# Performance work log

Measured on AMD Instinct MI355X. Metric: run time of the kernel, lower is better.

## Reference

```python
import jax, jax.numpy as jnp
import numpy as np

B, S, HIST = 2, 2048, 2048
H, HK, D = 16, 16, 128
DIM = H * D

def setup_inputs() -> dict:
    key = jax.random.key(0)
    ks = jax.random.split(key, 8)
    x = jax.random.normal(ks[0], (B, S, DIM), jnp.float32)
    prev_k = jax.random.normal(ks[1], (B, HIST, HK, D), jnp.float32)
    prev_v = jax.random.normal(ks[2], (B, HIST, HK, D), jnp.float32)
    # causal mask: history fully visible, causal within the current chunk
    q_pos = HIST + jnp.arange(S)
    k_pos = jnp.arange(HIST + S)
    mask = jnp.where(k_pos[None, :] <= q_pos[:, None], 0.0, -1e9).astype(jnp.float32)[None, None]
    sc = 0.02
    wq = jax.random.normal(ks[3], (DIM, DIM), jnp.float32) * sc
    wk = jax.random.normal(ks[4], (DIM, DIM), jnp.float32) * sc
    wv = jax.random.normal(ks[5], (DIM, DIM), jnp.float32) * sc
    wo = jax.random.normal(ks[6], (DIM, DIM), jnp.float32) * sc
    return {"x": x, "prev_k": prev_k, "prev_v": prev_v, "mask": mask,
            "wq": wq, "wk": wk, "wv": wv, "wo": wo}

def reference(x, prev_k, prev_v, mask, wq, wk, wv, wo):
    b, s, _ = x.shape
    # nn.Linear: y = x @ W^T, weights stored [out, in]
    xq = jnp.einsum('bsd,ed->bse', x, wq).reshape(b, s, H, D)
    xk = jnp.einsum('bsd,ed->bse', x, wk).reshape(b, s, HK, D)
    xv = jnp.einsum('bsd,ed->bse', x, wv).reshape(b, s, HK, D)
    k_all = jnp.concatenate([prev_k, xk], axis=1)  # [b, hist+s, hk, d]
    v_all = jnp.concatenate([prev_v, xv], axis=1)
    scores = jnp.einsum('bqhd,bkhd->bhqk', xq, k_all) / jnp.sqrt(jnp.float32(D))
    scores = scores + mask
    probs = jax.nn.softmax(scores.astype(jnp.float32), axis=-1).astype(xq.dtype)
    out = jnp.einsum('bhqk,bkhd->bqhd', probs, v_all).reshape(b, s, H * D)
    out = jnp.einsum('bse,de->bsd', out, wo)
    return out, k_all, v_all
```

## Files before the change

### kernel.cpp

```cpp
#include <hip/hip_runtime.h>
#include <math.h>

typedef __attribute__((ext_vector_type(8))) short bf16x8;
typedef __attribute__((ext_vector_type(4))) short bf16x4;
typedef __attribute__((ext_vector_type(4))) float f32x4;

#define SSCL (0.08838834764831845f * 1.4426950408889634f)

__device__ __forceinline__ short f2bf(float f) {
    union { float f; unsigned u; } x; x.f = f;
    unsigned r = x.u + 0x7fffu + ((x.u >> 16) & 1u);
    return (short)(r >> 16);
}
__device__ __forceinline__ float bf2f(short s) {
    union { unsigned u; float f; } x;
    x.u = ((unsigned)(unsigned short)s) << 16;
    return x.f;
}

typedef const __attribute__((address_space(1))) unsigned int* gas_ptr;
typedef __attribute__((address_space(3))) unsigned int* las_ptr;
__device__ __forceinline__ void async_copy16(const void* g, void* l) {
    __builtin_amdgcn_global_load_lds((gas_ptr)g, (las_ptr)l, 16, 0, 0);
}

__global__ __launch_bounds__(256)
void cvt_kernel(const float* __restrict__ src, short* __restrict__ dst, int n4) {
    int i = blockIdx.x * 256 + threadIdx.x;
    const int stride = gridDim.x * 256;
    for (; i < n4; i += stride) {
        float4 v = ((const float4*)src)[i];
        bf16x4 o;
        o[0] = f2bf(v.x); o[1] = f2bf(v.y); o[2] = f2bf(v.z); o[3] = f2bf(v.w);
        ((bf16x4*)dst)[i] = o;
    }
}

__global__ __launch_bounds__(256)
void cvt3_kernel(const float* __restrict__ s0, const float* __restrict__ s1,
                 const float* __restrict__ s2, short* __restrict__ d0,
                 short* __restrict__ d1, short* __restrict__ d2, int n4) {
    const float* src = (blockIdx.y == 0) ? s0 : ((blockIdx.y == 1) ? s1 : s2);
    short* dst = (blockIdx.y == 0) ? d0 : ((blockIdx.y == 1) ? d1 : d2);
    int i = blockIdx.x * 256 + threadIdx.x;
    const int stride = gridDim.x * 256;
    for (; i < n4; i += stride) {
        float4 v = ((const float4*)src)[i];
        bf16x4 o;
        o[0] = f2bf(v.x); o[1] = f2bf(v.y); o[2] = f2bf(v.z); o[3] = f2bf(v.w);
        ((bf16x4*)dst)[i] = o;
    }
}

template<int QKV>
__global__ __launch_bounds__(256)
void gemm_kernel(const short* __restrict__ A,
                 const short* __restrict__ B0, const short* __restrict__ B1,
                 const short* __restrict__ B2,
                 short* __restrict__ D16, float* __restrict__ Dk,
                 float* __restrict__ Dv, float* __restrict__ Df) {
    __shared__ short As[128 * 64];
    __shared__ short Bs[128 * 64];
    const int tid = threadIdx.x, w = tid >> 6, ln = tid & 63;
    const int col = ln & 15, quad = ln >> 4;
    const int sel = QKV ? (blockIdx.x >> 4) : 0;
    const int tn = (blockIdx.x & 15) * 128;
    const int tm = blockIdx.y * 128;
    const short* B = (sel == 0) ? B0 : ((sel == 1) ? B1 : B2);

    const int wm = (w >> 1) * 64, wn = (w & 1) * 64;
    const int srow = ln >> 3, scol = (ln & 7) * 8;

    f32x4 acc[4][4];
    for (int i = 0; i < 4; ++i)
        for (int j = 0; j < 4; ++j)
            for (int e = 0; e < 4; ++e) acc[i][j][e] = 0.f;

    for (int k0 = 0; k0 < 2048; k0 += 64) {
        #pragma unroll
        for (int i = 0; i < 4; ++i) {
            int chunk = i * 4 + w;
            int row = chunk * 8 + srow;
            async_copy16(&A[(tm + row) * 2048 + k0 + scol], &As[chunk * 512]);
            async_copy16(&B[(tn + row) * 2048 + k0 + scol], &Bs[chunk * 512]);
        }
        asm volatile("s_waitcnt vmcnt(0)" ::: "memory");
        __syncthreads();
        #pragma unroll
        for (int kk = 0; kk < 2; ++kk) {
            bf16x8 af[4], bfr[4];
            #pragma unroll
            for (int i = 0; i < 4; ++i)
                af[i] = *(const bf16x8*)&As[(wm + i * 16 + col) * 64 + kk * 32 + quad * 8];
            #pragma unroll
            for (int j = 0; j < 4; ++j)
                bfr[j] = *(const bf16x8*)&Bs[(wn + j * 16 + col) * 64 + kk * 32 + quad * 8];
            __builtin_amdgcn_s_setprio(1);
            #pragma unroll
            for (int i = 0; i < 4; ++i)
                #pragma unroll
                for (int j = 0; j < 4; ++j)
                    acc[i][j] = __builtin_amdgcn_mfma_f32_16x16x32_bf16(af[i], bfr[j], acc[i][j], 0, 0, 0);
            __builtin_amdgcn_s_setprio(0);
        }
        __syncthreads();
    }
    for (int i = 0; i < 4; ++i)
        for (int j = 0; j < 4; ++j)
            for (int r = 0; r < 4; ++r) {
                int m = tm + wm + i * 16 + quad * 4 + r;
                int n = tn + wn + j * 16 + col;
                float v = acc[i][j][r];
                if (QKV) {
                    if (sel == 0) {
                        D16[m * 2048 + n] = f2bf(v);
                    } else {
                        int orow = m + ((m >> 11) + 1) * 2048;
                        float* D = (sel == 1) ? Dk : Dv;
                        D[orow * 2048 + n] = v;
                    }
                } else {
                    Df[m * 2048 + n] = v;
                }
            }
}

__global__ __launch_bounds__(256)
void prep_kv(const float* __restrict__ Kall, const float* __restrict__ Vall,
             short* __restrict__ Ktg, short* __restrict__ Vtg) {
    __shared__ short L[64 * 132];
    const int tid = threadIdx.x;
    const int k0 = blockIdx.x * 64;
    const int h = blockIdx.y, b = blockIdx.z;
    const float* Kb = Kall + ((size_t)(b * 4096) * 16 + h) * 128;
    const float* Vb = Vall + ((size_t)(b * 4096) * 16 + h) * 128;
    short* Ko = Ktg + ((size_t)(b * 16 + h) * 4096) * 128;
    short* Vo = Vtg + ((size_t)(b * 16 + h) * 128) * 4096;
    #pragma unroll
    for (int i = 0; i < 8; ++i) {
        int idx = i * 256 + tid;
        int kr = idx >> 5, c4 = (idx & 31) * 4;
        float4 v = *(const float4*)&Kb[(size_t)(k0 + kr) * 2048 + c4];
        bf16x4 o4;
        o4[0] = f2bf(v.x); o4[1] = f2bf(v.y); o4[2] = f2bf(v.z); o4[3] = f2bf(v.w);
        *(bf16x4*)&Ko[(size_t)(k0 + kr) * 128 + (c4 ^ ((kr & 7) << 3))] = o4;
    }
    #pragma unroll
    for (int i = 0; i < 8; ++i) {
        int idx = i * 256 + tid;
        int r = idx >> 5, c4 = (idx & 31) * 4;
        float4 v = *(const float4*)&Vb[(size_t)(k0 + r) * 2048 + c4];
        bf16x4 o4;
        o4[0] = f2bf(v.x); o4[1] = f2bf(v.y); o4[2] = f2bf(v.z); o4[3] = f2bf(v.w);
        *(bf16x4*)&L[r * 132 + c4] = o4;
    }
    __syncthreads();
    #pragma unroll
    for (int i = 0; i < 8; ++i) {
        int idx = i * 256 + tid;
        int d = idx >> 4, kc4 = (idx & 15) * 4;
        bf16x4 o4;
        o4[0] = L[(kc4 + 0) * 132 + d];
        o4[1] = L[(kc4 + 1) * 132 + d];
        o4[2] = L[(kc4 + 2) * 132 + d];
        o4[3] = L[(kc4 + 3) * 132 + d];
        *(bf16x4*)&Vo[(size_t)d * 4096 + k0 + (kc4 ^ ((d & 7) << 3))] = o4;
    }
}

__global__ __launch_bounds__(256)
void attn_mfma(const short* __restrict__ Q, const short* __restrict__ Ktg,
               const short* __restrict__ Vtg, short* __restrict__ Ot) {
    __shared__ short Ks[2][64 * 128];
    __shared__ short Vs[2][128 * 64];
    __shared__ short Ps[4 * 16 * 72];
    const int tid = threadIdx.x, w = tid >> 6, ln = tid & 63;
    const int col = ln & 15, quad = ln >> 4;
    const int bh = blockIdx.x;
    const int b = bh >> 4, h = bh & 15;
    const int s0 = blockIdx.y * 64;
    const int xk = (col & 7) << 3;

    bf16x8 qf[4];
    {
        const int qr = (b * 2048 + s0 + w * 16 + col) * 2048 + h * 128;
        #pragma unroll
        for (int ks = 0; ks < 4; ++ks)
            qf[ks] = *(const bf16x8*)&Q[qr + ks * 32 + quad * 8];
    }
    f32x4 o[8];
    #pragma unroll
    for (int i = 0; i < 8; ++i)
        for (int e = 0; e < 4; ++e) o[i][e] = 0.f;
    float mr[4] = {-1e30f, -1e30f, -1e30f, -1e30f};
    float lr[4] = {0.f, 0.f, 0.f, 0.f};

    const short* Kb = Ktg + ((size_t)(b * 16 + h) * 4096) * 128;
    const short* Vb = Vtg + ((size_t)(b * 16 + h) * 128) * 4096;
    short* PsW = &Ps[w * 1152];

    const int kr4 = ln >> 4;
    const int kc8 = (ln & 15) * 8;
    const int vd = (ln >> 3);
    const int vkofs = (ln & 7) * 8;

    const int ntiles = 33 + blockIdx.y;

    #pragma unroll
    for (int i = 0; i < 4; ++i) {
        int ch = i * 4 + w;
        async_copy16(&Kb[(size_t)(ch * 4 + kr4) * 128 + kc8], &Ks[0][ch * 512]);
        async_copy16(&Vb[(size_t)(ch * 8 + vd) * 4096 + vkofs], &Vs[0][ch * 512]);
    }
    asm volatile("s_waitcnt vmcnt(0)" ::: "memory");
    __syncthreads();

    for (int t = 0; t < ntiles; ++t) {
        const int p = t & 1;
        const int k0 = t * 64;
        const bool pf = (t + 1 < ntiles);

        if (pf) {
            const int k0n = k0 + 64;
            #pragma unroll
            for (int i = 0; i < 4; ++i) {
                int ch = i * 4 + w;
                async_copy16(&Kb[(size_t)(k0n + ch * 4 + kr4) * 128 + kc8],
                             &Ks[p ^ 1][ch * 512]);
                async_copy16(&Vb[(size_t)(ch * 8 + vd) * 4096 + k0n + vkofs],
                             &Vs[p ^ 1][ch * 512]);
            }
        }

        f32x4 s4[4];
        #pragma unroll
        for (int j = 0; j < 4; ++j)
            for (int e = 0; e < 4; ++e) s4[j][e] = 0.f;
        #pragma unroll
        for (int ks = 0; ks < 4; ++ks) {
            const int dofs = (ks * 32 + quad * 8) ^ xk;
            bf16x8 kf[4];
            #pragma unroll
            for (int j = 0; j < 4; ++j)
                kf[j] = *(const bf16x8*)&Ks[p][(j * 16 + col) * 128 + dofs];
            __builtin_amdgcn_s_setprio(1);
            #pragma unroll
            for (int j = 0; j < 4; ++j)
                s4[j] = __builtin_amdgcn_mfma_f32_16x16x32_bf16(qf[ks], kf[j], s4[j], 0, 0, 0);
            __builtin_amdgcn_s_setprio(0);
        }

        const bool full = (k0 + 63 <= 2048 + s0 + w * 16);
        float pp[4][4];
        if (full) {
            #pragma unroll
            for (int j = 0; j < 4; ++j)
                #pragma unroll
                for (int r = 0; r < 4; ++r) pp[j][r] = s4[j][r] * SSCL;
        } else {
            #pragma unroll
            for (int j = 0; j < 4; ++j) {
                int kp = k0 + j * 16 + col;
                #pragma unroll
                for (int r = 0; r < 4; ++r) {
                    int qp = 2048 + s0 + w * 16 + quad * 4 + r;
                    pp[j][r] = (kp <= qp) ? s4[j][r] * SSCL : -1e30f;
                }
            }
        }
        #pragma unroll
        for (int r = 0; r < 4; ++r) {
            float mx = fmaxf(fmaxf(pp[0][r], pp[1][r]), fmaxf(pp[2][r], pp[3][r]));
            mx = fmaxf(mx, __shfl_xor(mx, 1));
            mx = fmaxf(mx, __shfl_xor(mx, 2));
            mx = fmaxf(mx, __shfl_xor(mx, 4));
            mx = fmaxf(mx, __shfl_xor(mx, 8));
            float mn = fmaxf(mr[r], mx);
            float al = exp2f(mr[r] - mn);
            mr[r] = mn;
            float rs = 0.f;
            #pragma unroll
            for (int j = 0; j < 4; ++j) { pp[j][r] = exp2f(pp[j][r] - mn); rs += pp[j][r]; }
            rs += __shfl_xor(rs, 1);
            rs += __shfl_xor(rs, 2);
            rs += __shfl_xor(rs, 4);
            rs += __shfl_xor(rs, 8);
            lr[r] = lr[r] * al + rs;
            #pragma unroll
            for (int i = 0; i < 8; ++i) o[i][r] *= al;
        }
        #pragma unroll
        for (int j = 0; j < 4; ++j)
            #pragma unroll
            for (int r = 0; r < 4; ++r)
                PsW[(quad * 4 + r) * 72 + j * 16 + col] = f2bf(pp[j][r]);
        bf16x8 pa0 = *(const bf16x8*)&PsW[col * 72 + quad * 8];
        bf16x8 pa1 = *(const bf16x8*)&PsW[col * 72 + 32 + quad * 8];
        #pragma unroll
        for (int dt = 0; dt < 8; ++dt) {
            int row = dt * 16 + col;
            bf16x8 v0 = *(const bf16x8*)&Vs[p][row * 64 + ((quad * 8) ^ xk)];
            bf16x8 v1 = *(const bf16x8*)&Vs[p][row * 64 + ((32 + quad * 8) ^ xk)];
            __builtin_amdgcn_s_setprio(1);
            o[dt] = __builtin_amdgcn_mfma_f32_16x16x32_bf16(pa0, v0, o[dt], 0, 0, 0);
            o[dt] = __builtin_amdgcn_mfma_f32_16x16x32_bf16(pa1, v1, o[dt], 0, 0, 0);
            __builtin_amdgcn_s_setprio(0);
        }

        asm volatile("s_waitcnt vmcnt(0)" ::: "memory");
        __syncthreads();
    }
    const int orow = (b * 2048 + s0 + w * 16) * 2048 + h * 128;
    #pragma unroll
    for (int r = 0; r < 4; ++r) {
        float inv = 1.f / lr[r];
        #pragma unroll
        for (int dt = 0; dt < 8; ++dt)
            Ot[orow + (quad * 4 + r) * 2048 + dt * 16 + col] = f2bf(o[dt][r] * inv);
    }
}

extern "C" void kernel_launch(void* const* d_in, const int* in_sizes, int n_in,
                              void* d_out, int out_size, void* d_ws, size_t ws_size,
                              hipStream_t stream) {
    const float* x  = (const float*)d_in[0];
    const float* pk = (const float*)d_in[1];
    const float* pv = (const float*)d_in[2];
    const float* wq = (const float*)d_in[4];
    const float* wk = (const float*)d_in[5];
    const float* wv = (const float*)d_in[6];
    const float* wo = (const float*)d_in[7];

    float* out  = (float*)d_out;
    float* kall = out + 8388608;
    float* vall = out + 25165824;

    short* ws16 = (short*)d_ws;
    short* xb  = ws16;
    short* wqb = ws16 + 8388608;
    short* wkb = ws16 + 12582912;
    short* wvb = ws16 + 16777216;
    short* wob = ws16 + 20971520;
    short* vtg = ws16 + 8388608;
    short* qbf = ws16 + 25165824;
    short* ot  = xb;
    short* ktg = (short*)out;

    hipMemcpyAsync(kall,           pk,           16777216u, hipMemcpyDeviceToDevice, stream);
    hipMemcpyAsync(kall + 8388608, pk + 4194304, 16777216u, hipMemcpyDeviceToDevice, stream);
    hipMemcpyAsync(vall,           pv,           16777216u, hipMemcpyDeviceToDevice, stream);
    hipMemcpyAsync(vall + 8388608, pv + 4194304, 16777216u, hipMemcpyDeviceToDevice, stream);

    cvt_kernel<<<1024, 256, 0, stream>>>(x, xb, 2097152);
    cvt3_kernel<<<dim3(512, 3), 256, 0, stream>>>(wq, wk, wv, wqb, wkb, wvb, 1048576);

    gemm_kernel<1><<<dim3(48, 32), 256, 0, stream>>>(xb, wqb, wkb, wvb,
                                                     qbf, kall, vall, nullptr);
    prep_kv<<<dim3(64, 16, 2), 256, 0, stream>>>(kall, vall, ktg, vtg);
    attn_mfma<<<dim3(32, 32), 256, 0, stream>>>(qbf, ktg, vtg, ot);
    cvt_kernel<<<512, 256, 0, stream>>>(wo, wob, 1048576);
    gemm_kernel<0><<<dim3(16, 32), 256, 0, stream>>>(ot, wob, wob, wob,
                                                     nullptr, nullptr, nullptr, out);
}
```

Measured before the change: 834.8 us.

## Transpose QK^T MFMA so each lane owns one query row, skip rescale

Swaps MFMA operands so the score tile is K·Q^T, giving each lane a single query row (the column index). Row max and sum then need only two cross-lane shuffles instead of four per row, with one m/l scalar per lane. The softmax scale is folded into the Q projection epilogue, removing the per-score multiply. A wave-uniform branch skips the O rescale when no row max grows. The cost is shuffles to broadcast alpha and l back to the output layout, and P stores to LDS change to 4-element vectors.

Result: faster. 764.1 us (-8.5%).

```diff
diff --git a/kernel.cpp b/kernel.cpp
--- a/kernel.cpp
+++ b/kernel.cpp
@@ -11,11 +11,6 @@
     union { float f; unsigned u; } x; x.f = f;
     unsigned r = x.u + 0x7fffu + ((x.u >> 16) & 1u);
     return (short)(r >> 16);
-}
-__device__ __forceinline__ float bf2f(short s) {
-    union { unsigned u; float f; } x;
-    x.u = ((unsigned)(unsigned short)s) << 16;
-    return x.f;
 }
 
 typedef const __attribute__((address_space(1))) unsigned int* gas_ptr;
@@ -113,7 +108,7 @@
                 float v = acc[i][j][r];
                 if (QKV) {
                     if (sel == 0) {
-                        D16[m * 2048 + n] = f2bf(v);
+                        D16[m * 2048 + n] = f2bf(v * SSCL);
                     } else {
                         int orow = m + ((m >> 11) + 1) * 2048;
                         float* D = (sel == 1) ? Dk : Dv;
@@ -192,8 +187,7 @@
     #pragma unroll
     for (int i = 0; i < 8; ++i)
         for (int e = 0; e < 4; ++e) o[i][e] = 0.f;
-    float mr[4] = {-1e30f, -1e30f, -1e30f, -1e30f};
-    float lr[4] = {0.f, 0.f, 0.f, 0.f};
+    float m = -1e30f, l = 0.f;
 
     const short* Kb = Ktg + ((size_t)(b * 16 + h) * 4096) * 128;
     const short* Vb = Vtg + ((size_t)(b * 16 + h) * 128) * 4096;
@@ -205,6 +199,7 @@
     const int vkofs = (ln & 7) * 8;
 
     const int ntiles = 33 + blockIdx.y;
+    const int qp = 2048 + s0 + w * 16 + col;
 
     #pragma unroll
     for (int i = 0; i < 4; ++i) {
@@ -246,7 +241,7 @@
             __builtin_amdgcn_s_setprio(1);
             #pragma unroll
             for (int j = 0; j < 4; ++j)
-                s4[j] = __builtin_amdgcn_mfma_f32_16x16x32_bf16(qf[ks], kf[j], s4[j], 0, 0, 0);
+                s4[j] = __builtin_amdgcn_mfma_f32_16x16x32_bf16(kf[j], qf[ks], s4[j], 0, 0, 0);
             __builtin_amdgcn_s_setprio(0);
         }
 
@@ -256,44 +251,61 @@
             #pragma unroll
             for (int j = 0; j < 4; ++j)
                 #pragma unroll
-                for (int r = 0; r < 4; ++r) pp[j][r] = s4[j][r] * SSCL;
+                for (int r = 0; r < 4; ++r) pp[j][r] = s4[j][r];
         } else {
             #pragma unroll
             for (int j = 0; j < 4; ++j) {
-                int kp = k0 + j * 16 + col;
                 #pragma unroll
                 for (int r = 0; r < 4; ++r) {
-                    int qp = 2048 + s0 + w * 16 + quad * 4 + r;
-                    pp[j][r] = (kp <= qp) ? s4[j][r] * SSCL : -1e30f;
+                    int kp = k0 + j * 16 + quad * 4 + r;
+                    pp[j][r] = (kp <= qp) ? s4[j][r] : -1e30f;
                 }
             }
         }
-        #pragma unroll
-        for (int r = 0; r < 4; ++r) {
-            float mx = fmaxf(fmaxf(pp[0][r], pp[1][r]), fmaxf(pp[2][r], pp[3][r]));
-            mx = fmaxf(mx, __shfl_xor(mx, 1));
-            mx = fmaxf(mx, __shfl_xor(mx, 2));
-            mx = fmaxf(mx, __shfl_xor(mx, 4));
-            mx = fmaxf(mx, __shfl_xor(mx, 8));
-            float mn = fmaxf(mr[r], mx);
-            float al = exp2f(mr[r] - mn);
-            mr[r] = mn;
+        float mx = pp[0][0];
+        #pragma unroll
+        for (int j = 0; j < 4; ++j)
+            #pragma unroll
+            for (int r = 0; r < 4; ++r) mx = fmaxf(mx, pp[j][r]);
+        mx = fmaxf(mx, __shfl_xor(mx, 16));
+        mx = fmaxf(mx, __shfl_xor(mx, 32));
+
+        if (__all(mx <= m)) {
             float rs = 0.f;
             #pragma unroll
-            for (int j = 0; j < 4; ++j) { pp[j][r] = exp2f(pp[j][r] - mn); rs += pp[j][r]; }
-            rs += __shfl_xor(rs, 1);
-            rs += __shfl_xor(rs, 2);
-            rs += __shfl_xor(rs, 4);
-            rs += __shfl_xor(rs, 8);
-            lr[r] = lr[r] * al + rs;
-            #pragma unroll
-            for (int i = 0; i < 8; ++i) o[i][r] *= al;
-        }
-        #pragma unroll
-        for (int j = 0; j < 4; ++j)
-            #pragma unroll
-            for (int r = 0; r < 4; ++r)
-                PsW[(quad * 4 + r) * 72 + j * 16 + col] = f2bf(pp[j][r]);
+            for (int j = 0; j < 4; ++j)
+                #pragma unroll
+                for (int r = 0; r < 4; ++r) { pp[j][r] = exp2f(pp[j][r] - m); rs += pp[j][r]; }
+            rs += __shfl_xor(rs, 16);
+            rs += __shfl_xor(rs, 32);
+            l += rs;
+        } else {
+            float mn = fmaxf(m, mx);
+            float al = exp2f(m - mn);
+            m = mn;
+            float rs = 0.f;
+            #pragma unroll
+            for (int j = 0; j < 4; ++j)
+                #pragma unroll
+                for (int r = 0; r < 4; ++r) { pp[j][r] = exp2f(pp[j][r] - mn); rs += pp[j][r]; }
+            rs += __shfl_xor(rs, 16);
+            rs += __shfl_xor(rs, 32);
+            l = l * al + rs;
+            #pragma unroll
+            for (int r = 0; r < 4; ++r) {
+                float alr = __shfl(al, quad * 4 + r);
+                #pragma unroll
+                for (int i = 0; i < 8; ++i) o[i][r] *= alr;
+            }
+        }
+
+        #pragma unroll
+        for (int j = 0; j < 4; ++j) {
+            bf16x4 pb;
+            pb[0] = f2bf(pp[j][0]); pb[1] = f2bf(pp[j][1]);
+            pb[2] = f2bf(pp[j][2]); pb[3] = f2bf(pp[j][3]);
+            *(bf16x4*)&PsW[col * 72 + j * 16 + quad * 4] = pb;
+        }
         bf16x8 pa0 = *(const bf16x8*)&PsW[col * 72 + quad * 8];
         bf16x8 pa1 = *(const bf16x8*)&PsW[col * 72 + 32 + quad * 8];
         #pragma unroll
@@ -313,7 +325,7 @@
     const int orow = (b * 2048 + s0 + w * 16) * 2048 + h * 128;
     #pragma unroll
     for (int r = 0; r < 4; ++r) {
-        float inv = 1.f / lr[r];
+        float inv = 1.f / __shfl(l, quad * 4 + r);
         #pragma unroll
         for (int dt = 0; dt < 8; ++dt)
             Ot[orow + (quad * 4 + r) * 2048 + dt * 16 + col] = f2bf(o[dt][r] * inv);
```
